# Optimization experiments

Hardware: AMD Instinct MI355X
Metric: run time of the kernel (lower is better)

Reference implementation:

```python
import jax, jax.numpy as jnp
import numpy as np

B, IN, OUT = 4096, 1024, 1024


def setup_inputs() -> dict:
    key = jax.random.key(0)
    ks = jax.random.split(key, 11)
    xav = 1.0 / np.sqrt(IN + OUT)  # Xavier-style scale for sigmoid/tanh layers
    d = {
        "x": jax.random.normal(ks[0], (B, IN), dtype=jnp.float32),
        "h": jax.random.normal(ks[1], (B, OUT), dtype=jnp.float32),
        "c": jax.random.normal(ks[2], (B, OUT), dtype=jnp.float32),
        "w_f": jax.random.normal(ks[3], (IN + OUT, OUT), dtype=jnp.float32) * xav,
        "b_f": jnp.zeros((1, OUT), dtype=jnp.float32),
        "w_i": jax.random.normal(ks[4], (IN + OUT, OUT), dtype=jnp.float32) * xav,
        "b_i": jnp.zeros((1, OUT), dtype=jnp.float32),
        "w_c": jax.random.normal(ks[5], (IN + OUT, OUT), dtype=jnp.float32) * xav,
        "b_c": jnp.zeros((1, OUT), dtype=jnp.float32),
        "w_o": jax.random.normal(ks[6], (IN + OUT, OUT), dtype=jnp.float32) * xav,
        "b_o": jnp.zeros((1, OUT), dtype=jnp.float32),
    }
    return d


def reference(x, h, c, w_f, b_f, w_i, b_i, w_c, b_c, w_o, b_o):
    # combined input [B, IN+OUT]
    z = jnp.concatenate([x, h], axis=1)
    f = jax.nn.sigmoid(z @ w_f + b_f)      # forget gate
    i = jax.nn.sigmoid(z @ w_i + b_i)      # update (input) gate
    g = jnp.tanh(z @ w_c + b_c)            # candidate cell
    o = jax.nn.sigmoid(z @ w_o + b_o)      # output gate
    c_new = c * f + i * g
    h_new = jnp.tanh(c_new) * o
    return h_new
```

## Files before the change

kernel.cpp:

```cpp
#include <hip/hip_runtime.h>
#include <hip/hip_bf16.h>

typedef short short8 __attribute__((ext_vector_type(8)));
typedef float f32x16 __attribute__((ext_vector_type(16)));

#define NB 4096
#define KZ 2048
#define NG 1024
#define NKS 32

__device__ __forceinline__ unsigned short f2bf(float f) {
  unsigned int u = __float_as_uint(f);
  u += 0x7FFFu + ((u >> 16) & 1u);
  return (unsigned short)(u >> 16);
}
__device__ __forceinline__ float bf2f(unsigned short s) {
  return __uint_as_float(((unsigned int)s) << 16);
}
__device__ __forceinline__ void gload_lds16(const void* g, void* l) {
  __builtin_amdgcn_global_load_lds(
      (__attribute__((address_space(1))) void*)g,
      (__attribute__((address_space(3))) void*)l, 16, 0, 0);
}
__device__ __forceinline__ float sigm(float x) { return 1.f / (1.f + __expf(-x)); }
__device__ __forceinline__ float tanh_fast(float x) {
  float e = __expf(-2.f * fabsf(x));
  float r = (1.f - e) / (1.f + e);
  return copysignf(r, x);
}

__global__ void zsplit_kernel(const float* __restrict__ x, const float* __restrict__ h,
                              unsigned short* __restrict__ zh) {
  int idx = blockIdx.x * 256 + threadIdx.x;
  int e = idx << 2;
  int r = e >> 11;
  int k = e & (KZ - 1);
  const float* src = (k < 1024) ? (x + ((size_t)r << 10) + k)
                                : (h + ((size_t)r << 10) + (k - 1024));
  float4 v = *reinterpret_cast<const float4*>(src);
  float vf[4] = {v.x, v.y, v.z, v.w};
  unsigned short hh[4];
#pragma unroll
  for (int j = 0; j < 4; ++j) hh[j] = f2bf(vf[j]);
  uint2 H = make_uint2((unsigned)hh[0] | ((unsigned)hh[1] << 16),
                       (unsigned)hh[2] | ((unsigned)hh[3] << 16));
  *reinterpret_cast<uint2*>(zh + e) = H;
}

__global__ void wsplit_kernel(const float* __restrict__ w0, const float* __restrict__ w1,
                              const float* __restrict__ w2, const float* __restrict__ w3,
                              unsigned short* __restrict__ wh, unsigned short* __restrict__ wl) {
  __shared__ float tile[32][33];
  int g = blockIdx.z;
  const float* w = (g == 0) ? w0 : (g == 1) ? w1 : (g == 2) ? w2 : w3;
  int k0 = blockIdx.x << 5;
  int n0 = blockIdx.y << 5;
  int t = threadIdx.x;
  int rk = t >> 3, q = t & 7;
  float4 v = *reinterpret_cast<const float4*>(w + (size_t)(k0 + rk) * NG + n0 + (q << 2));
  tile[rk][(q << 2) + 0] = v.x;
  tile[rk][(q << 2) + 1] = v.y;
  tile[rk][(q << 2) + 2] = v.z;
  tile[rk][(q << 2) + 3] = v.w;
  __syncthreads();
  int n = t >> 3, kq = t & 7;
  unsigned short hs[4], ls[4];
#pragma unroll
  for (int j = 0; j < 4; ++j) {
    float f = tile[(kq << 2) + j][n];
    unsigned short hi = f2bf(f);
    unsigned short lo = f2bf(f - bf2f(hi));
    hs[j] = hi; ls[j] = lo;
  }
  int nn = n0 + n;
  int p = ((nn >> 6) << 8) | (((nn >> 4) & 3) << 6) | ((g >> 1) << 5) | ((g & 1) << 4) | (nn & 15);
  size_t o = (size_t)p * KZ + k0 + (kq << 2);
  uint2 H = make_uint2((unsigned)hs[0] | ((unsigned)hs[1] << 16),
                       (unsigned)hs[2] | ((unsigned)hs[3] << 16));
  uint2 L = make_uint2((unsigned)ls[0] | ((unsigned)ls[1] << 16),
                       (unsigned)ls[2] | ((unsigned)ls[3] << 16));
  *reinterpret_cast<uint2*>(wh + o) = H;
  *reinterpret_cast<uint2*>(wl + o) = L;
}

#define MFMA32(a, b, c) __builtin_amdgcn_mfma_f32_32x32x16_bf16((a), (b), (c), 0, 0, 0)
#define BAR() __builtin_amdgcn_s_barrier()
#define LGKM(N) asm volatile("s_waitcnt lgkmcnt(" #N ")" ::: "memory")
#define VMC0() asm volatile("s_waitcnt vmcnt(0)" ::: "memory")
#define SB() __builtin_amdgcn_sched_barrier(0)
#define PRIO1() __builtin_amdgcn_s_setprio(1)
#define PRIO0() __builtin_amdgcn_s_setprio(0)

__global__ __launch_bounds__(512, 2) void lstm_gemm256_kernel(
    const unsigned short* __restrict__ zh,
    const unsigned short* __restrict__ wh, const unsigned short* __restrict__ wl,
    const float* __restrict__ c_in, const float* __restrict__ bf_,
    const float* __restrict__ bi_, const float* __restrict__ bc_,
    const float* __restrict__ bo_, float* __restrict__ out) {
  __shared__ unsigned short As[2 * 16384];
  __shared__ unsigned short Bh[16384];
  __shared__ unsigned short Bl[16384];
  const int t = threadIdx.x;
  const int lane = t & 63;
  const int wid = t >> 6;
  const int wr = wid >> 2;
  const int wc = wid & 3;
  const int l31 = lane & 31;
  const int l5 = lane >> 5;

  const int bid = blockIdx.x;
  const int xcd = bid & 7;
  const int i = bid >> 3;
  const int bx = (xcd << 1) | (i & 1);
  const int by = i >> 1;
  const int brow0 = by << 8;
  const int pcol0 = bx << 8;

  char* AsB = (char*)As;
  char* BhB = (char*)Bh;
  char* BlB = (char*)Bl;

  int aoff[2], boff[2];
#pragma unroll
  for (int j = 0; j < 2; ++j) {
    int row = (j << 6) + (t >> 3);
    int sl = (t & 7) ^ (row & 7);
    aoff[j] = (brow0 + row) * KZ + (sl << 3);
    boff[j] = (pcol0 + row) * KZ + (sl << 3);
  }
  const int ldsw = wid << 10;

  auto STAGE = [&](int s, int hx) {
    if (s >= NKS) return;
    const int kk = s << 6;
    if (hx < 2) {
      const int lb = ((s & 1) << 15) + (hx << 14);
#pragma unroll
      for (int j = 0; j < 2; ++j)
        gload_lds16(zh + aoff[j] + hx * (128 * KZ) + kk, AsB + lb + (j << 13) + ldsw);
    } else if (hx < 4) {
      const int hq = hx - 2;
#pragma unroll
      for (int j = 0; j < 2; ++j)
        gload_lds16(wh + boff[j] + hq * (128 * KZ) + kk, BhB + (hq << 14) + (j << 13) + ldsw);
    } else {
      const int hq = hx - 4;
#pragma unroll
      for (int j = 0; j < 2; ++j)
        gload_lds16(wl + boff[j] + hq * (128 * KZ) + kk, BlB + (hq << 14) + (j << 13) + ldsw);
    }
  };

  f32x16 acc[4][2];
#pragma unroll
  for (int mt = 0; mt < 4; ++mt)
#pragma unroll
    for (int nt = 0; nt < 2; ++nt)
#pragma unroll
      for (int r = 0; r < 16; ++r) acc[mt][nt][r] = 0.f;

  const int rx = lane & 7;
  int sxk[4];
#pragma unroll
  for (int ks = 0; ks < 4; ++ks) sxk[ks] = (((ks << 1) + l5) ^ rx) << 4;
  const int aR = l31 << 7;
  const int aW = wr << 14;
  const int bWq = wc << 13;

  short8 aF0[4], aF1[4], bh0F[2], bh1F[2], bl0F[2], bl1F[2];

  STAGE(0, 0); STAGE(0, 1); STAGE(0, 2); STAGE(0, 3); STAGE(0, 4); STAGE(0, 5);
  VMC0();
  BAR();

  for (int m = 0; m < NKS; ++m) {
    const int abase = ((m & 1) << 15) + aW;

    auto RD = [&](short8* aF, short8* bhF, short8* blF, int sx) {
#pragma unroll
      for (int mt = 0; mt < 4; ++mt)
        aF[mt] = *reinterpret_cast<const short8*>(AsB + abase + (mt << 12) + aR + sx);
#pragma unroll
      for (int nt = 0; nt < 2; ++nt) {
        bhF[nt] = *reinterpret_cast<const short8*>(BhB + bWq + (nt << 12) + aR + sx);
        blF[nt] = *reinterpret_cast<const short8*>(BlB + bWq + (nt << 12) + aR + sx);
      }
    };
    auto MM = [&](const short8* aF, const short8* bF) {
#pragma unroll
      for (int mt = 0; mt < 4; ++mt)
#pragma unroll
        for (int nt = 0; nt < 2; ++nt)
          acc[mt][nt] = MFMA32(aF[mt], bF[nt], acc[mt][nt]);
    };

    STAGE(m + 1, 0); STAGE(m + 1, 1);

    RD(aF0, bh0F, bl0F, sxk[0]);
    SB();
    RD(aF1, bh1F, bl1F, sxk[1]);
    SB();
    LGKM(8); SB();
    PRIO1(); MM(aF0, bh0F); MM(aF0, bl0F); PRIO0();

    RD(aF0, bh0F, bl0F, sxk[2]);
    SB();
    LGKM(8); SB();
    PRIO1(); MM(aF1, bh1F); MM(aF1, bl1F); PRIO0();

    RD(aF1, bh1F, bl1F, sxk[3]);
    SB();
    LGKM(8); SB();
    PRIO1(); MM(aF0, bh0F); MM(aF0, bl0F); PRIO0();

    LGKM(0); SB();
    BAR();
    STAGE(m + 1, 2); STAGE(m + 1, 3);
    STAGE(m + 1, 4); STAGE(m + 1, 5);
    PRIO1(); MM(aF1, bh1F); MM(aF1, bl1F); PRIO0();
    VMC0(); SB();
    BAR();
  }

  const int c = lane & 15;
  const int gh = (lane >> 4) & 1;
  const int ng = (bx << 6) + (wc << 4) + c;
  const float vbf = bf_[ng], vbi = bi_[ng], vbc = bc_[ng], vbo = bo_[ng];
#pragma unroll
  for (int mt = 0; mt < 4; ++mt) {
    float oth0[16], oth1[16];
#pragma unroll
    for (int r = 0; r < 16; ++r) {
      oth0[r] = __shfl_xor(acc[mt][0][r], 16, 64);
      oth1[r] = __shfl_xor(acc[mt][1][r], 16, 64);
    }
#pragma unroll
    for (int r = 0; r < 16; ++r) {
      const int row = brow0 + (wr << 7) + (mt << 5) + (r & 3) + ((r >> 2) << 3) + (l5 << 2);
      const float fp = (gh ? oth0[r] : acc[mt][0][r]) + vbf;
      const float ip = (gh ? acc[mt][0][r] : oth0[r]) + vbi;
      const float gp = (gh ? oth1[r] : acc[mt][1][r]) + vbc;
      const float op = (gh ? acc[mt][1][r] : oth1[r]) + vbo;
      const float co = c_in[(size_t)row * NG + ng];
      const float cnew = co * sigm(fp) + sigm(ip) * tanh_fast(gp);
      out[(size_t)row * NG + ng] = tanh_fast(cnew) * sigm(op);
    }
  }
}

extern "C" void kernel_launch(void* const* d_in, const int* in_sizes, int n_in,
                              void* d_out, int out_size, void* d_ws, size_t ws_size,
                              hipStream_t stream) {
  const float* x   = (const float*)d_in[0];
  const float* h   = (const float*)d_in[1];
  const float* c   = (const float*)d_in[2];
  const float* w_f = (const float*)d_in[3];
  const float* b_f = (const float*)d_in[4];
  const float* w_i = (const float*)d_in[5];
  const float* b_i = (const float*)d_in[6];
  const float* w_c = (const float*)d_in[7];
  const float* b_c = (const float*)d_in[8];
  const float* w_o = (const float*)d_in[9];
  const float* b_o = (const float*)d_in[10];
  float* out = (float*)d_out;

  unsigned short* zh = (unsigned short*)d_ws;
  unsigned short* wh = zh + (size_t)NB * KZ;
  unsigned short* wl = wh + (size_t)KZ * 4096;

  zsplit_kernel<<<(NB * KZ / 4) / 256, 256, 0, stream>>>(x, h, zh);
  wsplit_kernel<<<dim3(KZ / 32, NG / 32, 4), 256, 0, stream>>>(w_f, w_i, w_c, w_o, wh, wl);
  lstm_gemm256_kernel<<<256, 512, 0, stream>>>(zh, wh, wl, c,
                                               b_f, b_i, b_c, b_o, out);
}
```

Measured before the change: 158.8 us.

## Switch GEMM to 128x256 tiles with 16x16x32 MFMA and triple-buffered B

Halves the row tile to 128, doubling the grid to 512 blocks so more CUs are busy. The GEMM now uses 16x16x32 bf16 MFMAs, and the weight layout is permuted so each lane's four accumulators hold the f/i/g/o gates directly, which removes the cross-lane shuffle in the epilogue. B (hi/lo weights) is staged in 32-wide k slices through a 3-deep LDS ring and A is double-buffered, with partial vmcnt waits so loads overlap compute. The cost is more A/B reloads per output element and smaller MFMA shapes, with per-step barriers.

```diff
diff --git a/kernel.cpp b/kernel.cpp
--- a/kernel.cpp
+++ b/kernel.cpp
@@ -2,12 +2,12 @@
 #include <hip/hip_bf16.h>
 
 typedef short short8 __attribute__((ext_vector_type(8)));
-typedef float f32x16 __attribute__((ext_vector_type(16)));
+typedef float f32x4 __attribute__((ext_vector_type(4)));
 
 #define NB 4096
 #define KZ 2048
 #define NG 1024
-#define NKS 32
+#define NSTEP 64
 
 __device__ __forceinline__ unsigned short f2bf(float f) {
   unsigned int u = __float_as_uint(f);
@@ -73,7 +73,7 @@
     hs[j] = hi; ls[j] = lo;
   }
   int nn = n0 + n;
-  int p = ((nn >> 6) << 8) | (((nn >> 4) & 3) << 6) | ((g >> 1) << 5) | ((g & 1) << 4) | (nn & 15);
+  int p = ((nn >> 6) << 8) | (((nn >> 4) & 3) << 6) | (g << 4) | (nn & 15);
   size_t o = (size_t)p * KZ + k0 + (kq << 2);
   uint2 H = make_uint2((unsigned)hs[0] | ((unsigned)hs[1] << 16),
                        (unsigned)hs[2] | ((unsigned)hs[3] << 16));
@@ -83,164 +83,147 @@
   *reinterpret_cast<uint2*>(wl + o) = L;
 }
 
-#define MFMA32(a, b, c) __builtin_amdgcn_mfma_f32_32x32x16_bf16((a), (b), (c), 0, 0, 0)
+#define MFMA(a, b, c) __builtin_amdgcn_mfma_f32_16x16x32_bf16((a), (b), (c), 0, 0, 0)
 #define BAR() __builtin_amdgcn_s_barrier()
 #define LGKM(N) asm volatile("s_waitcnt lgkmcnt(" #N ")" ::: "memory")
-#define VMC0() asm volatile("s_waitcnt vmcnt(0)" ::: "memory")
+#define VMC(N) asm volatile("s_waitcnt vmcnt(" #N ")" ::: "memory")
 #define SB() __builtin_amdgcn_sched_barrier(0)
 #define PRIO1() __builtin_amdgcn_s_setprio(1)
 #define PRIO0() __builtin_amdgcn_s_setprio(0)
 
-__global__ __launch_bounds__(512, 2) void lstm_gemm256_kernel(
+__global__ __launch_bounds__(512, 2) void lstm_gemm_kernel(
     const unsigned short* __restrict__ zh,
     const unsigned short* __restrict__ wh, const unsigned short* __restrict__ wl,
     const float* __restrict__ c_in, const float* __restrict__ bf_,
     const float* __restrict__ bi_, const float* __restrict__ bc_,
     const float* __restrict__ bo_, float* __restrict__ out) {
-  __shared__ unsigned short As[2 * 16384];
-  __shared__ unsigned short Bh[16384];
-  __shared__ unsigned short Bl[16384];
+  __shared__ unsigned short As[2 * 8192];
+  __shared__ unsigned short Bhs[3 * 8192];
+  __shared__ unsigned short Bls[3 * 8192];
   const int t = threadIdx.x;
   const int lane = t & 63;
   const int wid = t >> 6;
   const int wr = wid >> 2;
   const int wc = wid & 3;
-  const int l31 = lane & 31;
-  const int l5 = lane >> 5;
+  const int l15 = lane & 15;
+  const int l4 = lane >> 4;
 
   const int bid = blockIdx.x;
   const int xcd = bid & 7;
   const int i = bid >> 3;
-  const int bx = (xcd << 1) | (i & 1);
-  const int by = i >> 1;
-  const int brow0 = by << 8;
-  const int pcol0 = bx << 8;
+  const int bxc = (xcd << 1) | (i & 1);
+  const int byr = i >> 1;
+  const int brow0 = byr << 7;
+  const int pcol0 = bxc << 8;
 
   char* AsB = (char*)As;
-  char* BhB = (char*)Bh;
-  char* BlB = (char*)Bl;
-
-  int aoff[2], boff[2];
+  char* BhB = (char*)Bhs;
+  char* BlB = (char*)Bls;
+
+  int aoffA[2], boffB[2];
 #pragma unroll
   for (int j = 0; j < 2; ++j) {
-    int row = (j << 6) + (t >> 3);
-    int sl = (t & 7) ^ (row & 7);
-    aoff[j] = (brow0 + row) * KZ + (sl << 3);
-    boff[j] = (pcol0 + row) * KZ + (sl << 3);
-  }
-  const int ldsw = wid << 10;
-
-  auto STAGE = [&](int s, int hx) {
-    if (s >= NKS) return;
-    const int kk = s << 6;
-    if (hx < 2) {
-      const int lb = ((s & 1) << 15) + (hx << 14);
-#pragma unroll
-      for (int j = 0; j < 2; ++j)
-        gload_lds16(zh + aoff[j] + hx * (128 * KZ) + kk, AsB + lb + (j << 13) + ldsw);
-    } else if (hx < 4) {
-      const int hq = hx - 2;
-#pragma unroll
-      for (int j = 0; j < 2; ++j)
-        gload_lds16(wh + boff[j] + hq * (128 * KZ) + kk, BhB + (hq << 14) + (j << 13) + ldsw);
+    int ra = (j << 6) + (t >> 3);
+    aoffA[j] = (brow0 + ra) * KZ + (((t & 7) ^ (ra & 7)) << 3);
+    int rb2 = (j << 7) + (t >> 2);
+    boffB[j] = (pcol0 + rb2) * KZ + (((t & 3) ^ ((rb2 >> 1) & 3)) << 3);
+  }
+
+  auto STAGE_A = [&](int m) {
+    const int p = (m & 1) << 14;
+    const int kb = m << 6;
+#pragma unroll
+    for (int j = 0; j < 2; ++j)
+      gload_lds16(zh + aoffA[j] + kb, AsB + p + (j << 13) + (t << 4));
+  };
+  auto STAGE_B = [&](int s, int b) {
+    const int kb = s << 5;
+    const int bb = b << 14;
+#pragma unroll
+    for (int j = 0; j < 2; ++j) {
+      gload_lds16(wh + boffB[j] + kb, BhB + bb + (j << 13) + (t << 4));
+      gload_lds16(wl + boffB[j] + kb, BlB + bb + (j << 13) + (t << 4));
+    }
+  };
+
+  f32x4 acc[4][4];
+#pragma unroll
+  for (int mt = 0; mt < 4; ++mt)
+#pragma unroll
+    for (int nf = 0; nf < 4; ++nf) acc[mt][nf] = (f32x4){0.f, 0.f, 0.f, 0.f};
+
+  const int rxA = l15 & 7;
+  const int aRow = (wr << 13) + (l15 << 7);
+  const int sxB = (l4 ^ ((l15 >> 1) & 3)) << 4;
+  const int bRow = (wc << 12) + (l15 << 6) + sxB;
+
+  short8 a[4], bh[4], bl[4];
+
+  STAGE_A(0); STAGE_B(0, 0); STAGE_B(1, 1);
+  VMC(4);
+  BAR();
+
+  int rb = 0, sb = 2;
+  for (int s = 0; s < NSTEP; ++s) {
+    const int h = s & 1;
+    const int ap = ((s >> 1) & 1) << 14;
+    const int sxA = (((h << 2) + l4) ^ rxA) << 4;
+    const int bbase = rb << 14;
+
+#pragma unroll
+    for (int mt = 0; mt < 4; ++mt)
+      a[mt] = *reinterpret_cast<const short8*>(AsB + ap + aRow + (mt << 11) + sxA);
+#pragma unroll
+    for (int nf = 0; nf < 4; ++nf)
+      bh[nf] = *reinterpret_cast<const short8*>(BhB + bbase + bRow + (nf << 10));
+    SB();
+#pragma unroll
+    for (int nf = 0; nf < 4; ++nf)
+      bl[nf] = *reinterpret_cast<const short8*>(BlB + bbase + bRow + (nf << 10));
+    SB();
+
+    if (s < NSTEP - 2) {
+      STAGE_B(s + 2, sb);
+      if (h == 0) STAGE_A((s >> 1) + 1);
+    }
+
+    LGKM(4); SB();
+    PRIO1();
+#pragma unroll
+    for (int mt = 0; mt < 4; ++mt)
+#pragma unroll
+      for (int nf = 0; nf < 4; ++nf) acc[mt][nf] = MFMA(a[mt], bh[nf], acc[mt][nf]);
+    PRIO0();
+    LGKM(0); SB();
+    PRIO1();
+#pragma unroll
+    for (int mt = 0; mt < 4; ++mt)
+#pragma unroll
+      for (int nf = 0; nf < 4; ++nf) acc[mt][nf] = MFMA(a[mt], bl[nf], acc[mt][nf]);
+    PRIO0();
+
+    if (s < NSTEP - 2) {
+      if (h) { VMC(4); } else { VMC(6); }
     } else {
-      const int hq = hx - 4;
-#pragma unroll
-      for (int j = 0; j < 2; ++j)
-        gload_lds16(wl + boff[j] + hq * (128 * KZ) + kk, BlB + (hq << 14) + (j << 13) + ldsw);
-    }
-  };
-
-  f32x16 acc[4][2];
-#pragma unroll
-  for (int mt = 0; mt < 4; ++mt)
-#pragma unroll
-    for (int nt = 0; nt < 2; ++nt)
-#pragma unroll
-      for (int r = 0; r < 16; ++r) acc[mt][nt][r] = 0.f;
-
-  const int rx = lane & 7;
-  int sxk[4];
-#pragma unroll
-  for (int ks = 0; ks < 4; ++ks) sxk[ks] = (((ks << 1) + l5) ^ rx) << 4;
-  const int aR = l31 << 7;
-  const int aW = wr << 14;
-  const int bWq = wc << 13;
-
-  short8 aF0[4], aF1[4], bh0F[2], bh1F[2], bl0F[2], bl1F[2];
-
-  STAGE(0, 0); STAGE(0, 1); STAGE(0, 2); STAGE(0, 3); STAGE(0, 4); STAGE(0, 5);
-  VMC0();
-  BAR();
-
-  for (int m = 0; m < NKS; ++m) {
-    const int abase = ((m & 1) << 15) + aW;
-
-    auto RD = [&](short8* aF, short8* bhF, short8* blF, int sx) {
-#pragma unroll
-      for (int mt = 0; mt < 4; ++mt)
-        aF[mt] = *reinterpret_cast<const short8*>(AsB + abase + (mt << 12) + aR + sx);
-#pragma unroll
-      for (int nt = 0; nt < 2; ++nt) {
-        bhF[nt] = *reinterpret_cast<const short8*>(BhB + bWq + (nt << 12) + aR + sx);
-        blF[nt] = *reinterpret_cast<const short8*>(BlB + bWq + (nt << 12) + aR + sx);
-      }
-    };
-    auto MM = [&](const short8* aF, const short8* bF) {
-#pragma unroll
-      for (int mt = 0; mt < 4; ++mt)
-#pragma unroll
-        for (int nt = 0; nt < 2; ++nt)
-          acc[mt][nt] = MFMA32(aF[mt], bF[nt], acc[mt][nt]);
-    };
-
-    STAGE(m + 1, 0); STAGE(m + 1, 1);
-
-    RD(aF0, bh0F, bl0F, sxk[0]);
+      VMC(0);
+    }
     SB();
-    RD(aF1, bh1F, bl1F, sxk[1]);
-    SB();
-    LGKM(8); SB();
-    PRIO1(); MM(aF0, bh0F); MM(aF0, bl0F); PRIO0();
-
-    RD(aF0, bh0F, bl0F, sxk[2]);
-    SB();
-    LGKM(8); SB();
-    PRIO1(); MM(aF1, bh1F); MM(aF1, bl1F); PRIO0();
-
-    RD(aF1, bh1F, bl1F, sxk[3]);
-    SB();
-    LGKM(8); SB();
-    PRIO1(); MM(aF0, bh0F); MM(aF0, bl0F); PRIO0();
-
-    LGKM(0); SB();
     BAR();
-    STAGE(m + 1, 2); STAGE(m + 1, 3);
-    STAGE(m + 1, 4); STAGE(m + 1, 5);
-    PRIO1(); MM(aF1, bh1F); MM(aF1, bl1F); PRIO0();
-    VMC0(); SB();
-    BAR();
-  }
-
-  const int c = lane & 15;
-  const int gh = (lane >> 4) & 1;
-  const int ng = (bx << 6) + (wc << 4) + c;
+    rb = (rb == 2) ? 0 : rb + 1;
+    sb = (sb == 2) ? 0 : sb + 1;
+  }
+
+  const int ng = (bxc << 6) + (wc << 4) + l15;
   const float vbf = bf_[ng], vbi = bi_[ng], vbc = bc_[ng], vbo = bo_[ng];
 #pragma unroll
   for (int mt = 0; mt < 4; ++mt) {
-    float oth0[16], oth1[16];
-#pragma unroll
-    for (int r = 0; r < 16; ++r) {
-      oth0[r] = __shfl_xor(acc[mt][0][r], 16, 64);
-      oth1[r] = __shfl_xor(acc[mt][1][r], 16, 64);
-    }
-#pragma unroll
-    for (int r = 0; r < 16; ++r) {
-      const int row = brow0 + (wr << 7) + (mt << 5) + (r & 3) + ((r >> 2) << 3) + (l5 << 2);
-      const float fp = (gh ? oth0[r] : acc[mt][0][r]) + vbf;
-      const float ip = (gh ? acc[mt][0][r] : oth0[r]) + vbi;
-      const float gp = (gh ? oth1[r] : acc[mt][1][r]) + vbc;
-      const float op = (gh ? acc[mt][1][r] : oth1[r]) + vbo;
+#pragma unroll
+    for (int r = 0; r < 4; ++r) {
+      const int row = brow0 + (wr << 6) + (mt << 4) + (l4 << 2) + r;
+      const float fp = acc[mt][0][r] + vbf;
+      const float ip = acc[mt][1][r] + vbi;
+      const float gp = acc[mt][2][r] + vbc;
+      const float op = acc[mt][3][r] + vbo;
       const float co = c_in[(size_t)row * NG + ng];
       const float cnew = co * sigm(fp) + sigm(ip) * tanh_fast(gp);
       out[(size_t)row * NG + ng] = tanh_fast(cnew) * sigm(op);
@@ -270,6 +253,6 @@
 
   zsplit_kernel<<<(NB * KZ / 4) / 256, 256, 0, stream>>>(x, h, zh);
   wsplit_kernel<<<dim3(KZ / 32, NG / 32, 4), 256, 0, stream>>>(w_f, w_i, w_c, w_o, wh, wl);
-  lstm_gemm256_kernel<<<256, 512, 0, stream>>>(zh, wh, wl, c,
-                                               b_f, b_i, b_c, b_o, out);
-}
+  lstm_gemm_kernel<<<512, 512, 0, stream>>>(zh, wh, wl, c,
+                                            b_f, b_i, b_c, b_o, out);
+}
```

New measurement: 151.6 us. 1.05x faster.
